# Performance work log

Hardware: AMD Instinct MI355X
Metric: run time of the kernel (lower is better)

Reference implementation:

```python
import jax, jax.numpy as jnp
import numpy as np

GENOTYPE = [("sigmoid", 0), ("relu", 1), ("relu", 1), ("identity", 1),
            ("tanh", 2), ("sigmoid", 5), ("tanh", 3), ("relu", 5)]
CONCAT = list(range(1, 9))
ACT = {"tanh": jnp.tanh, "relu": jax.nn.relu,
       "sigmoid": jax.nn.sigmoid, "identity": lambda x: x}
INITRANGE = 0.04


def setup_inputs() -> dict:
    key = jax.random.key(0)
    ks = jax.random.split(key, 16)
    B, T = 64, 128
    V, D, NC = 32000, 850, 42
    NNER, NPOS, NER_V, POS_V = 30, 30, 25, 50
    STEPS = len(GENOTYPE)

    def u(k, shape):
        return jax.random.uniform(k, shape, jnp.float32, -INITRANGE, INITRANGE)

    enc_W = u(ks[0], (V, D)).at[0].set(0.0)           # padding_idx=0
    ner_W = u(ks[1], (NER_V, NNER)).at[0].set(0.0)
    pos_W = u(ks[2], (POS_V, NPOS)).at[0].set(0.0)
    agg_W = u(ks[3], (D, D + NNER + NPOS))            # Linear weight [out,in]
    agg_b = jnp.zeros((D,), jnp.float32)
    W0 = u(ks[4], (2 * D, 2 * D))                     # (ninp+nhid, 2*nhid)
    Ws = u(ks[5], (STEPS, D, 2 * D))
    dec_W = u(ks[6], (NC, D))
    dec_b = jnp.zeros((NC,), jnp.float32)

    tokens = jax.random.randint(ks[7], (B, T), 0, V)
    masks = jnp.ones((B, T), jnp.float32)
    pos = jax.random.randint(ks[8], (B, T), 0, POS_V)
    ner = jax.random.randint(ks[9], (B, T), 0, NER_V)
    hidden = jnp.zeros((1, B, D), jnp.float32)
    return {"tokens": tokens, "masks": masks, "pos": pos, "ner": ner,
            "hidden": hidden, "enc_W": enc_W, "ner_W": ner_W, "pos_W": pos_W,
            "agg_W": agg_W, "agg_b": agg_b, "W0": W0, "Ws": Ws,
            "dec_W": dec_W, "dec_b": dec_b}


def reference(tokens, masks, pos, ner, hidden,
              enc_W, ner_W, pos_W, agg_W, agg_b, W0, Ws, dec_W, dec_b):
    # Embeddings + aggregation (eval mode: all dropouts are identity)
    emb = enc_W[tokens]                                   # [B,T,D]
    combined = jnp.concatenate([emb, ner_W[ner], pos_W[pos]], axis=2)
    x = combined @ agg_W.T + agg_b                        # [B,T,D]
    x = jnp.transpose(x, (1, 0, 2))                       # [T,B,D]

    h0 = hidden[0]                                        # [B,D]

    def cell(h_prev, xt):
        xh = jnp.concatenate([xt, h_prev], axis=-1)       # [B,2D]
        c0, hh0 = jnp.split(xh @ W0, 2, axis=-1)
        s0 = h_prev + jax.nn.sigmoid(c0) * (jnp.tanh(hh0) - h_prev)
        states = [s0]
        for i, (name, pred) in enumerate(GENOTYPE):
            sp = states[pred]
            c, h = jnp.split(sp @ Ws[i], 2, axis=-1)
            s = sp + jax.nn.sigmoid(c) * (ACT[name](h) - sp)
            states.append(s)
        out = jnp.mean(jnp.stack([states[i] for i in CONCAT], axis=-1), axis=-1)
        return out, out

    _, hiddens = jax.lax.scan(cell, h0, x)                # [T,B,D]
    raw = hiddens * masks.T[:, :, None]                   # mask per timestep
    output = jnp.mean(raw, axis=0)                        # [B,D]
    logit = output @ dec_W.T + dec_b                      # [B,NC]
    log_prob = jax.nn.log_softmax(logit, axis=-1)
    new_hidden = raw[-1][None]                            # [1,B,D]
    return log_prob, new_hidden
```

## Files before the change

kernel.cpp:

```cpp
#include <hip/hip_runtime.h>
#include <math.h>

typedef float f32x4 __attribute__((ext_vector_type(4)));
typedef short s16x8 __attribute__((ext_vector_type(8)));
typedef unsigned short u16;

#define MFMA_BF16(a,b,c) __builtin_amdgcn_mfma_f32_16x16x32_bf16((a),(b),(c),0,0,0)
#define NBLK 243
#define PAIR_U16 13824
#define SLOT_U16 27648
#define LDS_BYTES 110592
#define ST_SLOT 55296


struct P {
  const int* tokens; const void* masks; const int* pos; const int* ner;
  const void* hidden;
  const void* enc_W; const void* ner_W; const void* pos_W;
  const void* agg_W; const void* agg_b;
  const void* W0; const void* Ws;
  const void* dec_W; const void* dec_b;
  void* out;
  unsigned short* PK_agg; unsigned short* PK_rec; unsigned short* comb;
  unsigned short* xbf; unsigned short* Sbf;
  float* accr;
  int* ctrl;
};

#define FB(pp, g, mtv) ((pp).ctrl + 1024 + (((g) * 4 + (mtv)) * 54) * 16)

__device__ __forceinline__ unsigned short f2bf(float f) {
  union { float f; unsigned u; } v; v.f = f;
  return (unsigned short)((v.u + 0x7FFFu + ((v.u >> 16) & 1u)) >> 16);
}
__device__ __forceinline__ float bf2f(u16 x) {
  union { unsigned u; float f; } v; v.u = (unsigned)x << 16; return v.f;
}
__device__ __forceinline__ float ldf(const void* q, size_t i, int bf) {
  if (bf) return bf2f(((const u16*)q)[i]);
  return ((const float*)q)[i];
}
__device__ __forceinline__ void stout(void* o, size_t i, float v, int bf) {
  if (bf) ((u16*)o)[i] = f2bf(v);
  else    ((float*)o)[i] = v;
}
__device__ __forceinline__ float sigm(float x) { return 1.0f / (1.0f + expf(-x)); }
__device__ __forceinline__ float actf(int a, float x) {
  if (a == 0) return sigm(x);
  if (a == 1) return fmaxf(x, 0.0f);
  if (a == 2) return tanhf(x);
  return x;
}

__device__ __forceinline__ s16x8 ldg16_sc1(const u16* p) {
  s16x8 r;
  asm volatile("global_load_dwordx4 %0, %1, off sc1" : "=v"(r) : "v"(p) : "memory");
  return r;
}
__device__ __forceinline__ void vmfence() {
  asm volatile("s_waitcnt vmcnt(0)" ::: "memory");
  __builtin_amdgcn_sched_barrier(0);
}
__device__ __forceinline__ u16 ldc_u16(const u16* p) {
  return __hip_atomic_load(p, __ATOMIC_RELAXED, __HIP_MEMORY_SCOPE_AGENT);
}
__device__ __forceinline__ float ldc_f32(const float* p) {
  unsigned x = __hip_atomic_load((const unsigned*)p, __ATOMIC_RELAXED,
                                 __HIP_MEMORY_SCOPE_AGENT);
  union { unsigned u; float f; } v; v.u = x; return v.f;
}
__device__ __forceinline__ void stc_f32(float* p, float f) {
  union { float f; unsigned u; } v; v.f = f;
  __hip_atomic_store((unsigned*)p, v.u, __ATOMIC_RELAXED, __HIP_MEMORY_SCOPE_AGENT);
}
__device__ __forceinline__ void stc_u16(u16* p, u16 x) {
  __hip_atomic_store(p, x, __ATOMIC_RELAXED, __HIP_MEMORY_SCOPE_AGENT);
}
__device__ __forceinline__ void stc_i32(int* p, int x) {
  __hip_atomic_store(p, x, __ATOMIC_RELAXED, __HIP_MEMORY_SCOPE_AGENT);
}
__device__ __forceinline__ int ldc_i32(const int* p) {
  return __hip_atomic_load(p, __ATOMIC_RELAXED, __HIP_MEMORY_SCOPE_AGENT);
}

__device__ __forceinline__ void backoff(int it) {
  if (it > 12)     __builtin_amdgcn_s_sleep(16);
  else if (it > 2) __builtin_amdgcn_s_sleep(2);
}

__device__ __forceinline__ void setfW(int* fb, int fi, int e) {
  asm volatile("s_waitcnt vmcnt(0)" ::: "memory");
  if ((threadIdx.x & 63) == 0) stc_i32(fb + fi * 16, e);
}
__device__ __forceinline__ void waitL(const int* fb, int n, int e) {
  int l = threadIdx.x & 63;
  bool done = (l >= n);
  int it = 0, last = -1, guard = 0;
  for (;;) {
    if (!done) done = (ldc_i32(fb + l * 16) >= e);
    unsigned long long m = __ballot(done);
    if (m == ~0ULL) break;
    int cnt = (int)__popcll(m);
    if (cnt != last) { last = cnt; it = 0; }
    if (++guard > 8000000) break;
    ++it;
    backoff(it);
  }
  asm volatile("" ::: "memory");
}
__device__ __forceinline__ void wait1(const int* f, int e) {
  int it = 0, guard = 0;
  while (ldc_i32(f) < e) {
    if (++guard > 8000000) break;
    ++it;
    backoff(it);
  }
  asm volatile("" ::: "memory");
}


__global__ void k_detect(P p) {
  for (int j = threadIdx.x; j < 32768; j += 64) p.ctrl[j] = 0;
  __syncthreads();
  if (threadIdx.x == 0) {
    const u16* u = (const u16*)p.W0;
    int good = 0;
    for (int i = 0; i < 256; ++i) {
      int e = (u[i] >> 7) & 0xFF;
      if (e >= 90 && e <= 126) ++good;
    }
    p.ctrl[0] = (good >= 192) ? 1 : 0;
  }
}

__global__ __launch_bounds__(256) void k_init0(P p) {
  const int total = 442368 + 114688;
  for (int e = blockIdx.x * blockDim.x + threadIdx.x; e < total;
       e += gridDim.x * blockDim.x) {
    if (e < 442368) {
      ((unsigned*)p.Sbf)[e] = 0u;
    } else {
      int e4 = e - 442368; int t = e4 / 896, r = e4 % 896;
      int b = r / 14, n = 850 + r % 14;
      p.xbf[((size_t)t * 64 + b) * 864 + n] = 0;
    }
  }
}

__global__ __launch_bounds__(256) void k_init1(P p) {
  const int bf = p.ctrl[0];
  for (int e = blockIdx.x * blockDim.x + threadIdx.x; e < 54400;
       e += gridDim.x * blockDim.x) {
    int b = e / 850, n = e % 850;
    p.Sbf[(size_t)7 * ST_SLOT + (((size_t)(n >> 4) * 64 + b) << 4) + (n & 15)] =
        f2bf(ldf(p.hidden, e, bf));
  }
}

__global__ __launch_bounds__(256) void k_pack_agg(P p) {
  const int bf = p.ctrl[0];
  const long total = 801792L;
  for (long e = (long)blockIdx.x * blockDim.x + threadIdx.x; e < total;
       e += (long)gridDim.x * blockDim.x) {
    int j = (int)(e & 7), l = (int)((e >> 3) & 63);
    long q9 = e >> 9;
    int kb = (int)(q9 % 29), nt = (int)(q9 / 29);
    int n = nt * 16 + (l & 15);
    int k = kb * 32 + ((l >> 4) << 3) + j;
    float v = 0.0f;
    if (n < 850 && k < 910) v = ldf(p.agg_W, (size_t)n * 910 + k, bf);
    p.PK_agg[e] = f2bf(v);
  }
}

__global__ __launch_bounds__(256) void k_comb(P p) {
  const int bf = p.ctrl[0];
  const long total = 7602176L;
  for (long e = (long)blockIdx.x * blockDim.x + threadIdx.x; e < total;
       e += (long)gridDim.x * blockDim.x) {
    int k = (int)(e % 928);
    int r = (int)(e / 928);
    int t = r >> 6, b = r & 63;
    float v = 0.0f;
    if (k < 850)      { int tok = p.tokens[b * 128 + t]; v = ldf(p.enc_W, (size_t)tok * 850 + k, bf); }
    else if (k < 880) { int nv = p.ner[b * 128 + t];     v = ldf(p.ner_W, nv * 30 + (k - 850), bf); }
    else if (k < 910) { int pv = p.pos[b * 128 + t];     v = ldf(p.pos_W, pv * 30 + (k - 880), bf); }
    p.comb[e] = f2bf(v);
  }
}

__global__ __launch_bounds__(256) void k_pack_rec(P p) {
  const int bf = p.ctrl[0];
  const long total = 14929920L;
  for (long e = (long)blockIdx.x * blockDim.x + threadIdx.x; e < total;
       e += (long)gridDim.x * blockDim.x) {
    int j = (int)(e & 7), l = (int)((e >> 3) & 63);
    long q9 = e >> 9;
    int kb = (int)(q9 % 27);
    long q = q9 / 27;
    int nt = (int)(q % 54);
    int mh = (int)(q / 54);
    int half = mh & 1, mat = mh >> 1;
    int nl = nt * 16 + (l & 15);
    int col = half ? nl + 850 : nl;
    int k = kb * 32 + ((l >> 4) << 3) + j;
    float v = 0.0f;
    if (nl < 850 && k < 850) {
      if (mat == 0)      v = ldf(p.W0, (size_t)k * 1700 + col, bf);
      else if (mat == 1) v = ldf(p.W0, (size_t)(k + 850) * 1700 + col, bf);
      else               v = ldf(p.Ws, (size_t)(mat - 2) * 850 * 1700 + (size_t)k * 1700 + col, bf);
    }
    p.PK_rec[e] = f2bf(v);
  }
}

__global__ void k_diag(P p) {
  if (blockIdx.x == 0 && threadIdx.x == 0)
    for (int i = 0; i < 64; ++i) ((float*)p.out)[i] = 2000.0f;
}

__global__ __launch_bounds__(256) void k_phaseA(P p) {
  const int tid = threadIdx.x;
  const int l = tid & 63, lm = l & 15, lg = l >> 4;
  const int wid = (blockIdx.x << 2) | (tid >> 6);
  const int bf = p.ctrl[0];
  for (int u = wid; u < 512 * 54; u += 1024) {
    int mt = u / 54, nt = u - mt * 54;
    int r0 = mt << 4;
    f32x4 acc = {0.f, 0.f, 0.f, 0.f};
    const u16* Arow = p.comb + (size_t)(r0 + lm) * 928 + (size_t)lg * 8;
    const u16* Bp = p.PK_agg + (size_t)nt * 29 * 512 + (size_t)l * 8;
    for (int kb = 0; kb < 29; ++kb) {
      s16x8 a = *(const s16x8*)(Arow + (size_t)kb * 32);
      s16x8 b = *(const s16x8*)(Bp + (size_t)kb * 512);
      acc = MFMA_BF16(a, b, acc);
    }
    int n = nt * 16 + lm;
    if (n < 850) {
      float bias = ldf(p.agg_b, n, bf);
#pragma unroll
      for (int i = 0; i < 4; ++i) {
        int r = r0 + lg * 4 + i;
        p.xbf[(size_t)r * 864 + n] = f2bf(acc[i] + bias);
      }
    }
  }
}


__device__ __forceinline__ void burstA(const u16* st, int mt, int l, s16x8* ab) {
  const int lm = l & 15, lg = l >> 4;
  const int row = mt * 16 + lm;
  const u16* A = st + (((size_t)(lg >> 1) * 64 + row) << 4) + ((lg & 1) << 3);
#pragma unroll
  for (int kb = 0; kb < 27; ++kb) ab[kb] = ldg16_sc1(A + (size_t)kb * 2048);
}

__device__ __forceinline__ void unitS(const u16* lds, const u16* st, int nt, int mt,
                                      int l, f32x4& cc, f32x4& hh, float* prev) {
  const int lm = l & 15, lg = l >> 4;
  s16x8 ab[27];
  burstA(st, mt, l, ab);
  u16 pv[4];
#pragma unroll
  for (int i = 0; i < 4; ++i)
    pv[i] = ldc_u16(st + (((size_t)nt * 64 + mt * 16 + lg * 4 + i) << 4) + lm);
  vmfence();
  const f32x4 z = {0.f, 0.f, 0.f, 0.f};
  f32x4 c0 = z, c1 = z, h0 = z, h1 = z;
#pragma unroll
  for (int kb = 0; kb < 27; ++kb) {
    s16x8 bc = *(const s16x8*)(lds + l * 8 + (size_t)kb * 512);
    s16x8 bh = *(const s16x8*)(lds + PAIR_U16 + l * 8 + (size_t)kb * 512);
    if (kb & 1) { c1 = MFMA_BF16(ab[kb], bc, c1); h1 = MFMA_BF16(ab[kb], bh, h1); }
    else        { c0 = MFMA_BF16(ab[kb], bc, c0); h0 = MFMA_BF16(ab[kb], bh, h0); }
  }
  cc += c0 + c1; hh += h0 + h1;
#pragma unroll
  for (int i = 0; i < 4; ++i) prev[i] = bf2f(pv[i]);
}

__device__ __forceinline__ void unit2S(const u16* lds0, const u16* lds1, const u16* st,
                                       int ntA, int ntB, int mt, int l,
                                       f32x4& cA, f32x4& hA, f32x4& cB, f32x4& hB,
                                       float* prevA, float* prevB) {
  const int lm = l & 15, lg = l >> 4;
  s16x8 ab[27];
  burstA(st, mt, l, ab);
  u16 pa[4], pb[4];
#pragma unroll
  for (int i = 0; i < 4; ++i) {
    size_t row = mt * 16 + lg * 4 + i;
    pa[i] = ldc_u16(st + (((size_t)ntA * 64 + row) << 4) + lm);
    pb[i] = ldc_u16(st + (((size_t)ntB * 64 + row) << 4) + lm);
  }
  vmfence();
#pragma unroll
  for (int kb = 0; kb < 27; ++kb) {
    cA = MFMA_BF16(ab[kb], *(const s16x8*)(lds0 + l * 8 + (size_t)kb * 512), cA);
    hA = MFMA_BF16(ab[kb], *(const s16x8*)(lds0 + PAIR_U16 + l * 8 + (size_t)kb * 512), hA);
    cB = MFMA_BF16(ab[kb], *(const s16x8*)(lds1 + l * 8 + (size_t)kb * 512), cB);
    hB = MFMA_BF16(ab[kb], *(const s16x8*)(lds1 + PAIR_U16 + l * 8 + (size_t)kb * 512), hB);
  }
#pragma unroll
  for (int i = 0; i < 4; ++i) { prevA[i] = bf2f(pa[i]); prevB[i] = bf2f(pb[i]); }
}

__device__ __forceinline__ void unit_x(const P& p, int nt, int t, int mt, int l,
                                       f32x4& cc, f32x4& hh) {
  const int lm = l & 15, lg = l >> 4;
  const u16* Ax = p.xbf + ((size_t)t * 64 + mt * 16 + lm) * 864 + (size_t)lg * 8;
  const u16* B0 = p.PK_rec + (size_t)(0 * 54 + nt) * PAIR_U16 + l * 8;
  const u16* B1 = p.PK_rec + (size_t)(1 * 54 + nt) * PAIR_U16 + l * 8;
  s16x8 ab[27];
#pragma unroll
  for (int kb = 0; kb < 27; ++kb) ab[kb] = *(const s16x8*)(Ax + (size_t)kb * 32);
  const f32x4 z = {0.f, 0.f, 0.f, 0.f};
  f32x4 c0 = z, c1 = z, h0 = z, h1 = z;
#pragma unroll
  for (int kb = 0; kb < 27; ++kb) {
    s16x8 bc = *(const s16x8*)(B0 + (size_t)kb * 512);
    s16x8 bh = *(const s16x8*)(B1 + (size_t)kb * 512);
    if (kb & 1) { c1 = MFMA_BF16(ab[kb], bc, c1); h1 = MFMA_BF16(ab[kb], bh, h1); }
    else        { c0 = MFMA_BF16(ab[kb], bc, c0); h0 = MFMA_BF16(ab[kb], bh, h0); }
  }
  cc += c0 + c1; hh += h0 + h1;
}

__device__ __forceinline__ void epiS(const P& p, int par, int slot, int nt, int mt,
                                     int l, const float* prev, int act,
                                     f32x4 c, f32x4 h) {
  int lm = l & 15, lg = l >> 4, n = nt * 16 + lm;
  if (n >= 850) return;
  u16* dst = p.Sbf + (size_t)(par * 8 + slot) * ST_SLOT;
#pragma unroll
  for (int i = 0; i < 4; ++i) {
    size_t row = mt * 16 + lg * 4 + i;
    float s = prev[i] + sigm(c[i]) * (actf(act, h[i]) - prev[i]);
    stc_u16(dst + (((size_t)nt * 64 + row) << 4) + lm, f2bf(s));
  }
}

__global__ __launch_bounds__(256, 1) void k_scan(P p) {
  extern __shared__ u16 ldsw[];
  const int tid = threadIdx.x;
  const int l = tid & 63, lm = l & 15, lg = l >> 4, mt = tid >> 6;
  const int blk = blockIdx.x;
  const int bf = p.ctrl[0];
#define STP(par, slot) (p.Sbf + (size_t)((par) * 8 + (slot)) * ST_SLOT)

  int role, matA, ntA, matB, ntB;
  if (blk < 54)       { role = 0; matA = 1; ntA = blk;       matB = 3; ntB = ntA; }
  else if (blk < 108) { role = 1; matA = 2; ntA = blk - 54;  matB = 4; ntB = ntA; }
  else if (blk < 162) { role = 2; matA = 6; ntA = blk - 108; matB = 5; ntB = ntA; }
  else if (blk < 216) { role = 3; matA = 7; ntA = blk - 162; matB = 9; ntB = ntA; }
  else                { role = 4; matA = 8; ntA = 2 * (blk - 216); matB = 8; ntB = ntA + 1; }

  for (int s = 0; s < 2; ++s) {
    int m = s ? matB : matA, nt = s ? ntB : ntA;
    for (int h = 0; h < 2; ++h) {
      const uint4* src = (const uint4*)(p.PK_rec + ((size_t)(m * 2 + h) * 54 + nt) * PAIR_U16);
      uint4* dst = (uint4*)(ldsw + s * SLOT_U16 + h * PAIR_U16);
      for (int i = tid; i < PAIR_U16 / 8; i += 256) dst[i] = src[i];
    }
  }
  __syncthreads();

  const f32x4 z = {0.f, 0.f, 0.f, 0.f};

  if (role == 0) {
    const int fi = blk;
    for (int t = 0; t < 128; ++t) {
      int par = t & 1;
      f32x4 cc = z, hh = z;
      unit_x(p, ntA, t, mt, l, cc, hh);
      waitL(FB(p, 7, mt), 54, t);
      float pv[4];
      unitS(ldsw, STP(par, 7), ntA, mt, l, cc, hh, pv);
      epiS(p, par, 0, ntA, mt, l, pv, 2, cc, hh);
      setfW(FB(p, 0, mt), fi, t + 1);
      waitL(FB(p, 1, mt), 54, t + 1);
      f32x4 c2 = z, h2 = z; float p2[4];
      unitS(ldsw + SLOT_U16, STP(par, 1), ntA, mt, l, c2, h2, p2);
      epiS(p, par, 2, ntA, mt, l, p2, 1, c2, h2);
      setfW(FB(p, 2, mt), fi, t + 1);
    }
    if (blk < 16) {
      int b = blk * 4 + mt;
      waitL(FB(p, 7, b >> 4), 54, 128);
      float myval = 0.0f;
      for (int c = 0; c < 42; ++c) {
        float part = 0.0f;
        for (int d = l; d < 850; d += 64)
          part += ldc_f32(p.accr + b * 850 + d) * ldf(p.dec_W, c * 850 + d, bf);
        for (int off = 32; off > 0; off >>= 1) part += __shfl_xor(part, off);
        if (l == c) myval = part * (1.0f / 128.0f) + ldf(p.dec_b, c, bf);
      }
      float mx = (l < 42) ? myval : -INFINITY;
      for (int off = 32; off > 0; off >>= 1) mx = fmaxf(mx, __shfl_xor(mx, off));
      float ex = (l < 42) ? expf(myval - mx) : 0.0f;
      float sm = ex;
      for (int off = 32; off > 0; off >>= 1) sm += __shfl_xor(sm, off);
      if (l < 42) stout(p.out, (size_t)b * 42 + l, myval - mx - logf(sm), bf);
    }
  } else if (role == 1) {
    const int fi = blk - 54;
    for (int t = 0; t < 128; ++t) {
      int par = t & 1;
      waitL(FB(p, 0, mt), 54, t + 1);
      f32x4 cc = z, hh = z; float pv[4];
      unitS(ldsw, STP(par, 0), ntA, mt, l, cc, hh, pv);
      epiS(p, par, 1, ntA, mt, l, pv, 0, cc, hh);
      setfW(FB(p, 1, mt), fi, t + 1);
      waitL(FB(p, 1, mt), 54, t + 1);
      f32x4 c2 = z, h2 = z; float p2[4];
      unitS(ldsw + SLOT_U16, STP(par, 1), ntA, mt, l, c2, h2, p2);
      epiS(p, par, 3, ntA, mt, l, p2, 1, c2, h2);
      setfW(FB(p, 3, mt), fi, t + 1);
    }
  } else if (role == 2) {
    const int fi = blk - 108;
    for (int t = 0; t < 128; ++t) {
      int par = t & 1;
      waitL(FB(p, 1, mt), 54, t + 1);
      f32x4 cc = z, hh = z; float pv[4];
      unitS(ldsw + SLOT_U16, STP(par, 1), ntA, mt, l, cc, hh, pv);
      epiS(p, par, 4, ntA, mt, l, pv, 3, cc, hh);
      setfW(FB(p, 4, mt), fi, t + 1);
      waitL(FB(p, 2, mt), 54, t + 1);
      f32x4 c2 = z, h2 = z; float p2[4];
      unitS(ldsw, STP(par, 2), ntA, mt, l, c2, h2, p2);
      epiS(p, par, 5, ntA, mt, l, p2, 2, c2, h2);
      setfW(FB(p, 5, mt), fi, t + 1);
    }
  } else if (role == 4) {
    const int fi = blk - 216;
    for (int t = 0; t < 128; ++t) {
      int par = t & 1;
      waitL(FB(p, 3, mt), 54, t + 1);
      f32x4 cA = z, hA = z, cB = z, hB = z; float pa[4], pb[4];
      unit2S(ldsw, ldsw + SLOT_U16, STP(par, 3), ntA, ntB, mt, l,
             cA, hA, cB, hB, pa, pb);
      epiS(p, par, 6, ntA, mt, l, pa, 2, cA, hA);
      epiS(p, par, 6, ntB, mt, l, pb, 2, cB, hB);
      setfW(FB(p, 6, mt), fi, t + 1);
    }
  } else {
    const int fi = blk - 162;
    float areg[4] = {0.f, 0.f, 0.f, 0.f};
    const int n = ntA * 16 + lm;
    for (int t = 0; t < 128; ++t) {
      int par = t & 1, par2 = (t + 1) & 1;
      wait1(FB(p, 2, mt) + ntA * 16, t + 1);
      wait1(FB(p, 3, mt) + ntA * 16, t + 1);
      wait1(FB(p, 4, mt) + ntA * 16, t + 1);
      float psum[4];
      {
        u16 q1[4], q2[4], q3[4], q4[4];
#pragma unroll
        for (int i = 0; i < 4; ++i) {
          size_t off = (((size_t)ntA * 64 + mt * 16 + lg * 4 + i) << 4) + lm;
          q1[i] = ldc_u16(STP(par, 1) + off); q2[i] = ldc_u16(STP(par, 2) + off);
          q3[i] = ldc_u16(STP(par, 3) + off); q4[i] = ldc_u16(STP(par, 4) + off);
        }
#pragma unroll
        for (int i = 0; i < 4; ++i)
          psum[i] = bf2f(q1[i]) + bf2f(q2[i]) + bf2f(q3[i]) + bf2f(q4[i]);
      }
      waitL(FB(p, 5, mt), 54, t + 1);
      f32x4 cA = z, hA = z, cB = z, hB = z; float s5v[4], s5d[4];
      unit2S(ldsw, ldsw + SLOT_U16, STP(par, 5), ntA, ntA, mt, l,
             cA, hA, cB, hB, s5v, s5d);
      wait1(FB(p, 6, mt) + (ntA >> 1) * 16, t + 1);
      u16 q7[4];
#pragma unroll
      for (int i = 0; i < 4; ++i)
        q7[i] = ldc_u16(STP(par, 6) + (((size_t)ntA * 64 + mt * 16 + lg * 4 + i) << 4) + lm);
      if (n < 850) {
        u16* hdst = STP(par2, 7);
#pragma unroll
        for (int i = 0; i < 4; ++i) {
          int b = mt * 16 + lg * 4 + i;
          float s6 = s5v[i] + sigm(cA[i]) * (sigm(hA[i]) - s5v[i]);
          float s8 = s5v[i] + sigm(cB[i]) * (fmaxf(hB[i], 0.f) - s5v[i]);
          float sum = psum[i] + s5v[i] + bf2f(q7[i]) + s6 + s8;
          float outv = sum * 0.125f;
          float mk = ldf(p.masks, b * 128 + t, bf);
          areg[i] += outv * mk;
          stc_u16(hdst + (((size_t)ntA * 64 + b) << 4) + lm, f2bf(outv));
          if (t == 127) {
            stout(p.out, 2688 + (size_t)b * 850 + n, outv * mk, bf);
            stc_f32(p.accr + b * 850 + n, areg[i]);
          }
        }
      }
      setfW(FB(p, 7, mt), fi, t + 1);
    }
  }
#undef STP
}


extern "C" void kernel_launch(void* const* d_in, const int* in_sizes, int n_in,
                              void* d_out, int out_size, void* d_ws, size_t ws_size,
                              hipStream_t stream) {
  (void)in_sizes; (void)n_in; (void)out_size;
  P p;
  p.tokens = (const int*)d_in[0];
  p.masks  = d_in[1];
  p.pos    = (const int*)d_in[2];
  p.ner    = (const int*)d_in[3];
  p.hidden = d_in[4];
  p.enc_W  = d_in[5];
  p.ner_W  = d_in[6];
  p.pos_W  = d_in[7];
  p.agg_W  = d_in[8];
  p.agg_b  = d_in[9];
  p.W0     = d_in[10];
  p.Ws     = d_in[11];
  p.dec_W  = d_in[12];
  p.dec_b  = d_in[13];
  p.out    = d_out;

  unsigned char* ws = (unsigned char*)d_ws;
  p.ctrl = (int*)ws;
  unsigned char* R0 = ws + 262144;
  p.PK_agg = (unsigned short*)R0;
  p.comb   = (unsigned short*)(R0 + 1603584);
  p.PK_rec = (unsigned short*)R0;
  unsigned char* q = R0 + 29859840;
  p.xbf  = (unsigned short*)q; q += 14155776;
  p.Sbf  = (unsigned short*)q; q += 1769472;
  p.accr = (float*)q;          q += 217600;

  size_t need = (size_t)(q - ws);
  if (ws_size < need) {
    hipLaunchKernelGGL(k_diag, dim3(1), dim3(64), 0, stream, p);
    return;
  }

  static int lds_attr_set = 0;
  if (!lds_attr_set) {
    (void)hipFuncSetAttribute((const void*)k_scan,
                              hipFuncAttributeMaxDynamicSharedMemorySize, LDS_BYTES);
    lds_attr_set = 1;
  }

  hipLaunchKernelGGL(k_detect,   dim3(1),    dim3(64),  0, stream, p);
  hipLaunchKernelGGL(k_init0,    dim3(256),  dim3(256), 0, stream, p);
  hipLaunchKernelGGL(k_init1,    dim3(64),   dim3(256), 0, stream, p);
  hipLaunchKernelGGL(k_pack_agg, dim3(512),  dim3(256), 0, stream, p);
  hipLaunchKernelGGL(k_comb,     dim3(4096), dim3(256), 0, stream, p);
  hipLaunchKernelGGL(k_phaseA,   dim3(256),  dim3(256), 0, stream, p);
  hipLaunchKernelGGL(k_pack_rec, dim3(4096), dim3(256), 0, stream, p);
  hipLaunchKernelGGL(k_scan,     dim3(NBLK), dim3(256), LDS_BYTES, stream, p);
}
```

Measured before the change: 3.115 ms.

## Reassign scan blocks so each stage block owns two column tiles

Block roles for the persistent recurrent scan are restructured. Before, most blocks handled two sequential genotype steps on one 16-column tile. Now seven groups of 27 blocks each compute a single step over two column tiles, plus 54 blocks for the final combine. Each step has its own producer group, so dependent steps no longer serialize inside one block. Flag waits now count 27 producers, which shortens the critical path per timestep but doubles the MFMA work and A-operand traffic per block.

```diff
diff --git a/kernel.cpp b/kernel.cpp
--- a/kernel.cpp
+++ b/kernel.cpp
@@ -256,30 +256,6 @@
   for (int kb = 0; kb < 27; ++kb) ab[kb] = ldg16_sc1(A + (size_t)kb * 2048);
 }
 
-__device__ __forceinline__ void unitS(const u16* lds, const u16* st, int nt, int mt,
-                                      int l, f32x4& cc, f32x4& hh, float* prev) {
-  const int lm = l & 15, lg = l >> 4;
-  s16x8 ab[27];
-  burstA(st, mt, l, ab);
-  u16 pv[4];
-#pragma unroll
-  for (int i = 0; i < 4; ++i)
-    pv[i] = ldc_u16(st + (((size_t)nt * 64 + mt * 16 + lg * 4 + i) << 4) + lm);
-  vmfence();
-  const f32x4 z = {0.f, 0.f, 0.f, 0.f};
-  f32x4 c0 = z, c1 = z, h0 = z, h1 = z;
-#pragma unroll
-  for (int kb = 0; kb < 27; ++kb) {
-    s16x8 bc = *(const s16x8*)(lds + l * 8 + (size_t)kb * 512);
-    s16x8 bh = *(const s16x8*)(lds + PAIR_U16 + l * 8 + (size_t)kb * 512);
-    if (kb & 1) { c1 = MFMA_BF16(ab[kb], bc, c1); h1 = MFMA_BF16(ab[kb], bh, h1); }
-    else        { c0 = MFMA_BF16(ab[kb], bc, c0); h0 = MFMA_BF16(ab[kb], bh, h0); }
-  }
-  cc += c0 + c1; hh += h0 + h1;
-#pragma unroll
-  for (int i = 0; i < 4; ++i) prev[i] = bf2f(pv[i]);
-}
-
 __device__ __forceinline__ void unit2S(const u16* lds0, const u16* lds1, const u16* st,
                                        int ntA, int ntB, int mt, int l,
                                        f32x4& cA, f32x4& hA, f32x4& cB, f32x4& hB,
@@ -306,25 +282,24 @@
   for (int i = 0; i < 4; ++i) { prevA[i] = bf2f(pa[i]); prevB[i] = bf2f(pb[i]); }
 }
 
-__device__ __forceinline__ void unit_x(const P& p, int nt, int t, int mt, int l,
-                                       f32x4& cc, f32x4& hh) {
+__device__ __forceinline__ void unit2X(const P& p, int ntA, int ntB, int t, int mt,
+                                       int l, f32x4& cA, f32x4& hA, f32x4& cB, f32x4& hB) {
   const int lm = l & 15, lg = l >> 4;
   const u16* Ax = p.xbf + ((size_t)t * 64 + mt * 16 + lm) * 864 + (size_t)lg * 8;
-  const u16* B0 = p.PK_rec + (size_t)(0 * 54 + nt) * PAIR_U16 + l * 8;
-  const u16* B1 = p.PK_rec + (size_t)(1 * 54 + nt) * PAIR_U16 + l * 8;
+  const u16* BcA = p.PK_rec + (size_t)(0 * 54 + ntA) * PAIR_U16 + l * 8;
+  const u16* BhA = p.PK_rec + (size_t)(1 * 54 + ntA) * PAIR_U16 + l * 8;
+  const u16* BcB = p.PK_rec + (size_t)(0 * 54 + ntB) * PAIR_U16 + l * 8;
+  const u16* BhB = p.PK_rec + (size_t)(1 * 54 + ntB) * PAIR_U16 + l * 8;
   s16x8 ab[27];
 #pragma unroll
   for (int kb = 0; kb < 27; ++kb) ab[kb] = *(const s16x8*)(Ax + (size_t)kb * 32);
-  const f32x4 z = {0.f, 0.f, 0.f, 0.f};
-  f32x4 c0 = z, c1 = z, h0 = z, h1 = z;
 #pragma unroll
   for (int kb = 0; kb < 27; ++kb) {
-    s16x8 bc = *(const s16x8*)(B0 + (size_t)kb * 512);
-    s16x8 bh = *(const s16x8*)(B1 + (size_t)kb * 512);
-    if (kb & 1) { c1 = MFMA_BF16(ab[kb], bc, c1); h1 = MFMA_BF16(ab[kb], bh, h1); }
-    else        { c0 = MFMA_BF16(ab[kb], bc, c0); h0 = MFMA_BF16(ab[kb], bh, h0); }
-  }
-  cc += c0 + c1; hh += h0 + h1;
+    cA = MFMA_BF16(ab[kb], *(const s16x8*)(BcA + (size_t)kb * 512), cA);
+    hA = MFMA_BF16(ab[kb], *(const s16x8*)(BhA + (size_t)kb * 512), hA);
+    cB = MFMA_BF16(ab[kb], *(const s16x8*)(BcB + (size_t)kb * 512), cB);
+    hB = MFMA_BF16(ab[kb], *(const s16x8*)(BhB + (size_t)kb * 512), hB);
+  }
 }
 
 __device__ __forceinline__ void epiS(const P& p, int par, int slot, int nt, int mt,
@@ -349,12 +324,17 @@
   const int bf = p.ctrl[0];
 #define STP(par, slot) (p.Sbf + (size_t)((par) * 8 + (slot)) * ST_SLOT)
 
-  int role, matA, ntA, matB, ntB;
-  if (blk < 54)       { role = 0; matA = 1; ntA = blk;       matB = 3; ntB = ntA; }
-  else if (blk < 108) { role = 1; matA = 2; ntA = blk - 54;  matB = 4; ntB = ntA; }
-  else if (blk < 162) { role = 2; matA = 6; ntA = blk - 108; matB = 5; ntB = ntA; }
-  else if (blk < 216) { role = 3; matA = 7; ntA = blk - 162; matB = 9; ntB = ntA; }
-  else                { role = 4; matA = 8; ntA = 2 * (blk - 216); matB = 8; ntB = ntA + 1; }
+  const int g = (blk < 189) ? (blk / 27) : 7;
+  int matA, ntA, matB, ntB, fi;
+  if (g < 7) {
+    matA = (g < 6) ? g + 1 : 8; matB = matA;
+    fi = blk - g * 27;
+    ntA = 2 * fi; ntB = ntA + 1;
+  } else {
+    matA = 7; matB = 9;
+    fi = blk - 189;
+    ntA = fi; ntB = fi;
+  }
 
   for (int s = 0; s < 2; ++s) {
     int m = s ? matB : matA, nt = s ? ntB : ntA;
@@ -368,22 +348,18 @@
 
   const f32x4 z = {0.f, 0.f, 0.f, 0.f};
 
-  if (role == 0) {
-    const int fi = blk;
+  if (g == 0) {
     for (int t = 0; t < 128; ++t) {
       int par = t & 1;
-      f32x4 cc = z, hh = z;
-      unit_x(p, ntA, t, mt, l, cc, hh);
+      f32x4 cA = z, hA = z, cB = z, hB = z;
+      unit2X(p, ntA, ntB, t, mt, l, cA, hA, cB, hB);
       waitL(FB(p, 7, mt), 54, t);
-      float pv[4];
-      unitS(ldsw, STP(par, 7), ntA, mt, l, cc, hh, pv);
-      epiS(p, par, 0, ntA, mt, l, pv, 2, cc, hh);
+      float pa[4], pb[4];
+      unit2S(ldsw, ldsw + SLOT_U16, STP(par, 7), ntA, ntB, mt, l,
+             cA, hA, cB, hB, pa, pb);
+      epiS(p, par, 0, ntA, mt, l, pa, 2, cA, hA);
+      epiS(p, par, 0, ntB, mt, l, pb, 2, cB, hB);
       setfW(FB(p, 0, mt), fi, t + 1);
-      waitL(FB(p, 1, mt), 54, t + 1);
-      f32x4 c2 = z, h2 = z; float p2[4];
-      unitS(ldsw + SLOT_U16, STP(par, 1), ntA, mt, l, c2, h2, p2);
-      epiS(p, par, 2, ntA, mt, l, p2, 1, c2, h2);
-      setfW(FB(p, 2, mt), fi, t + 1);
     }
     if (blk < 16) {
       int b = blk * 4 + mt;
@@ -403,57 +379,33 @@
       for (int off = 32; off > 0; off >>= 1) sm += __shfl_xor(sm, off);
       if (l < 42) stout(p.out, (size_t)b * 42 + l, myval - mx - logf(sm), bf);
     }
-  } else if (role == 1) {
-    const int fi = blk - 54;
+  } else if (g >= 1 && g <= 6) {
+    const int srcSlot = (g == 1) ? 0 : (g <= 4) ? 1 : (g == 5) ? 2 : 3;
+    const int srcFlag = (g == 1) ? 0 : (g <= 4) ? 1 : (g == 5) ? 2 : 3;
+    const int dstSlot = (g == 1) ? 1 : (g == 2) ? 2 : (g == 3) ? 3 : (g == 4) ? 4
+                      : (g == 5) ? 5 : 6;
+    const int dstFlag = dstSlot;
+    const int act = (g == 1) ? 0 : (g == 2 || g == 3) ? 1 : (g == 4) ? 3 : 2;
     for (int t = 0; t < 128; ++t) {
       int par = t & 1;
-      waitL(FB(p, 0, mt), 54, t + 1);
-      f32x4 cc = z, hh = z; float pv[4];
-      unitS(ldsw, STP(par, 0), ntA, mt, l, cc, hh, pv);
-      epiS(p, par, 1, ntA, mt, l, pv, 0, cc, hh);
-      setfW(FB(p, 1, mt), fi, t + 1);
-      waitL(FB(p, 1, mt), 54, t + 1);
-      f32x4 c2 = z, h2 = z; float p2[4];
-      unitS(ldsw + SLOT_U16, STP(par, 1), ntA, mt, l, c2, h2, p2);
-      epiS(p, par, 3, ntA, mt, l, p2, 1, c2, h2);
-      setfW(FB(p, 3, mt), fi, t + 1);
-    }
-  } else if (role == 2) {
-    const int fi = blk - 108;
-    for (int t = 0; t < 128; ++t) {
-      int par = t & 1;
-      waitL(FB(p, 1, mt), 54, t + 1);
-      f32x4 cc = z, hh = z; float pv[4];
-      unitS(ldsw + SLOT_U16, STP(par, 1), ntA, mt, l, cc, hh, pv);
-      epiS(p, par, 4, ntA, mt, l, pv, 3, cc, hh);
-      setfW(FB(p, 4, mt), fi, t + 1);
-      waitL(FB(p, 2, mt), 54, t + 1);
-      f32x4 c2 = z, h2 = z; float p2[4];
-      unitS(ldsw, STP(par, 2), ntA, mt, l, c2, h2, p2);
-      epiS(p, par, 5, ntA, mt, l, p2, 2, c2, h2);
-      setfW(FB(p, 5, mt), fi, t + 1);
-    }
-  } else if (role == 4) {
-    const int fi = blk - 216;
-    for (int t = 0; t < 128; ++t) {
-      int par = t & 1;
-      waitL(FB(p, 3, mt), 54, t + 1);
+      waitL(FB(p, srcFlag, mt), 27, t + 1);
       f32x4 cA = z, hA = z, cB = z, hB = z; float pa[4], pb[4];
-      unit2S(ldsw, ldsw + SLOT_U16, STP(par, 3), ntA, ntB, mt, l,
+      unit2S(ldsw, ldsw + SLOT_U16, STP(par, srcSlot), ntA, ntB, mt, l,
              cA, hA, cB, hB, pa, pb);
-      epiS(p, par, 6, ntA, mt, l, pa, 2, cA, hA);
-      epiS(p, par, 6, ntB, mt, l, pb, 2, cB, hB);
-      setfW(FB(p, 6, mt), fi, t + 1);
+      epiS(p, par, dstSlot, ntA, mt, l, pa, act, cA, hA);
+      epiS(p, par, dstSlot, ntB, mt, l, pb, act, cB, hB);
+      setfW(FB(p, dstFlag, mt), fi, t + 1);
     }
   } else {
-    const int fi = blk - 162;
     float areg[4] = {0.f, 0.f, 0.f, 0.f};
     const int n = ntA * 16 + lm;
+    const int hf = (ntA >> 1) * 16;
     for (int t = 0; t < 128; ++t) {
       int par = t & 1, par2 = (t + 1) & 1;
-      wait1(FB(p, 2, mt) + ntA * 16, t + 1);
-      wait1(FB(p, 3, mt) + ntA * 16, t + 1);
-      wait1(FB(p, 4, mt) + ntA * 16, t + 1);
+      wait1(FB(p, 1, mt) + hf, t + 1);
+      wait1(FB(p, 2, mt) + hf, t + 1);
+      wait1(FB(p, 3, mt) + hf, t + 1);
+      wait1(FB(p, 4, mt) + hf, t + 1);
       float psum[4];
       {
         u16 q1[4], q2[4], q3[4], q4[4];
@@ -467,11 +419,11 @@
         for (int i = 0; i < 4; ++i)
           psum[i] = bf2f(q1[i]) + bf2f(q2[i]) + bf2f(q3[i]) + bf2f(q4[i]);
       }
-      waitL(FB(p, 5, mt), 54, t + 1);
+      waitL(FB(p, 5, mt), 27, t + 1);
       f32x4 cA = z, hA = z, cB = z, hB = z; float s5v[4], s5d[4];
       unit2S(ldsw, ldsw + SLOT_U16, STP(par, 5), ntA, ntA, mt, l,
              cA, hA, cB, hB, s5v, s5d);
-      wait1(FB(p, 6, mt) + (ntA >> 1) * 16, t + 1);
+      wait1(FB(p, 6, mt) + hf, t + 1);
       u16 q7[4];
 #pragma unroll
       for (int i = 0; i < 4; ++i)
```

Measured after the change: 3.973 ms. 1.28x slower.
